# Performance work log

Hardware: AMD Instinct MI355X
Metric: run time of the kernel (lower is better)

## Reference

```python
import jax, jax.numpy as jnp
import numpy as np

DIM = 128
HID = 4 * DIM  # hidden_rate=4
EPS = 1e-5     # torch LayerNorm default


def _ln(x, g, b):
    mu = jnp.mean(x, axis=-1, keepdims=True)
    var = jnp.mean(jnp.square(x - mu), axis=-1, keepdims=True)
    return (x - mu) * jax.lax.rsqrt(var + EPS) * g + b


def setup_inputs() -> dict:
    key = jax.random.key(0)
    ks = jax.random.split(key, 8)
    b, c, h, w = 4, DIM, 128, 128
    inp = {
        'inp_img': jax.random.normal(ks[0], (b, c, h, w), dtype=jnp.float32),
        # layer norms (gamma, beta)
        'ln0_g': jnp.ones((c,), jnp.float32), 'ln0_b': jnp.zeros((c,), jnp.float32),
        'ln1_g': jnp.ones((c,), jnp.float32), 'ln1_b': jnp.zeros((c,), jnp.float32),
        'ln2_g': jnp.ones((c,), jnp.float32), 'ln2_b': jnp.zeros((c,), jnp.float32),
        # SpatialMix output projection (out, in)
        'W_out': jax.random.normal(ks[1], (c, c), jnp.float32) * 0.05,
        # ChannelMix weights
        'W_whiten': jax.random.normal(ks[2], (c, c), jnp.float32) * 0.05,
        'W_key': jax.random.normal(ks[3], (HID, c), jnp.float32) * 0.05,
        'W_recep': jax.random.normal(ks[4], (c, c), jnp.float32) * 0.05,
        'W_value': jax.random.normal(ks[5], (c, HID), jnp.float32) * 0.05,
    }
    return inp


def _block(x, ln0_g, ln0_b, ln1_g, ln1_b, ln2_g, ln2_b,
           W_out, W_whiten, W_key, W_recep, W_value):
    # x: (b, c, h, w) -> tokens (b, T, c)
    b, c, h, w = x.shape
    t = x.reshape(b, c, h * w).transpose(0, 2, 1)
    # layer_id == 0 pre-norm
    t = _ln(t, ln0_g, ln0_b)
    # SpatialMix: jit_func output is discarded (sr overwritten with sigmoid(x));
    # effective math: output_proj(sigmoid(y) * y) on y = ln1(t)
    y1 = _ln(t, ln1_g, ln1_b)
    att = jnp.einsum('btc,oc->bto', jax.nn.sigmoid(y1) * y1, W_out)
    t = t + att
    # ChannelMix: for-else resets xk = xr = whitened x
    y2 = _ln(t, ln2_g, ln2_b)
    wht = jnp.einsum('btc,oc->bto', y2, W_whiten)                 # (b,T,c)
    k = jnp.square(jax.nn.relu(jnp.einsum('btc,hc->bth', wht, W_key)))  # (b,T,HID)
    kv = jnp.einsum('bth,ch->btc', k, W_value)                    # (b,T,c)
    r = jax.nn.sigmoid(jnp.einsum('btc,oc->bto', wht, W_recep))
    t = t + r * kv
    return t.transpose(0, 2, 1).reshape(b, c, h, w)


def reference(inp_img, ln0_g, ln0_b, ln1_g, ln1_b, ln2_g, ln2_b,
              W_out, W_whiten, W_key, W_recep, W_value):
    params = (ln0_g, ln0_b, ln1_g, ln1_b, ln2_g, ln2_b,
              W_out, W_whiten, W_key, W_recep, W_value)
    out1 = _block(inp_img, *params)
    # same encoder applied to h/w-transposed image, then transposed back
    out2 = _block(inp_img.transpose(0, 1, 3, 2), *params).transpose(0, 1, 3, 2)
    return out2 + out1
```

## Files before the change

kernel.cpp:

```cpp
#include <hip/hip_runtime.h>


#define HW    16384
#define CDIM  128
#define LDA   132
#define LDW   136
#define TPW   16
#define NW    16

#define OFF_OUT 0
#define OFF_WHT 16384
#define OFF_KEY 32768
#define OFF_REC 98304
#define OFF_VAL 114688
#define WS_ELEMS 180224

typedef __attribute__((ext_vector_type(8))) short short8;
typedef __attribute__((ext_vector_type(4))) float f32x4;

__device__ __forceinline__ float bf2f(ushort h) {
    union { uint u; float f; } v; v.u = ((uint)h) << 16; return v.f;
}
__device__ __forceinline__ ushort f2bf(float f) {
    union { float f; uint u; } v; v.f = f;
    uint u = v.u + 0x7fffu + ((v.u >> 16) & 1u);
    return (ushort)(u >> 16);
}
__device__ __forceinline__ float sigm(float x) {
    return 1.f / (1.f + __expf(-x));
}

__global__ void cvt_all(const float* __restrict__ Wout, const float* __restrict__ Wwht,
                        const float* __restrict__ Wkey, const float* __restrict__ Wrec,
                        const float* __restrict__ Wval, ushort* __restrict__ ws) {
    int i = blockIdx.x * 256 + threadIdx.x;
    float v;
    if      (i < 32768)  v = (i < 16384) ? Wout[i] : Wwht[i - 16384];
    else if (i < 98304)  v = Wkey[i - 32768];
    else if (i < 114688) v = Wrec[i - 98304];
    else                 v = Wval[i - 114688];
    ws[i] = f2bf(v);
}

template<bool PRE>
__device__ __forceinline__ void stageW(ushort* Wl,
                                       const ushort* __restrict__ wsrc,
                                       const float* __restrict__ fsrc,
                                       int src_ld, int row0, int k0, int tid) {
    const int rr = tid >> 4, cc = (tid & 15) * 8;
#pragma unroll
    for (int j = 0; j < 2; ++j) {
        const int r  = j * 64 + rr;
        const int si = (row0 + r) * src_ld + k0 + cc;
        if (PRE) {
            *(short8*)&Wl[r * LDW + cc] = *(const short8*)&wsrc[si];
        } else {
            const float* p = fsrc + si;
            float4 f0 = *(const float4*)p;
            float4 f1 = *(const float4*)(p + 4);
            union { ushort u[8]; short8 s; } t;
            t.u[0]=f2bf(f0.x); t.u[1]=f2bf(f0.y); t.u[2]=f2bf(f0.z); t.u[3]=f2bf(f0.w);
            t.u[4]=f2bf(f1.x); t.u[5]=f2bf(f1.y); t.u[6]=f2bf(f1.z); t.u[7]=f2bf(f1.w);
            *(short8*)&Wl[r * LDW + cc] = t.s;
        }
    }
}

__device__ __forceinline__ short8 ldA8(const ushort* p) {
    union { uint2 x[2]; short8 s; } r;
    r.x[0] = *(const uint2*)p;
    r.x[1] = *(const uint2*)(p + 4);
    return r.s;
}

__device__ __forceinline__ void gemm16(const ushort* A, const ushort* Wl,
                                       int q, int c, f32x4 acc[8]) {
#pragma unroll
    for (int kk = 0; kk < 4; ++kk) {
        short8 a = ldA8(A + c * LDA + kk * 32 + q * 8);
#pragma unroll
        for (int h = 0; h < 2; ++h) {
            short8 b[4];
#pragma unroll
            for (int g = 0; g < 4; ++g)
                b[g] = *(const short8*)&Wl[((h * 4 + g) * 16 + c) * LDW + kk * 32 + q * 8];
#pragma unroll
            for (int g = 0; g < 4; ++g)
                acc[h * 4 + g] = __builtin_amdgcn_mfma_f32_16x16x32_bf16(
                    a, b[g], acc[h * 4 + g], 0, 0, 0);
        }
    }
}

__device__ __forceinline__ void gemm8r(const short8* wa, const ushort* Wl,
                                       int nt0, int q, int c, f32x4 acc4[4]) {
#pragma unroll
    for (int kk = 0; kk < 4; ++kk) {
        short8 b[4];
#pragma unroll
        for (int g = 0; g < 4; ++g)
            b[g] = *(const short8*)&Wl[((nt0 + g) * 16 + c) * LDW + kk * 32 + q * 8];
#pragma unroll
        for (int g = 0; g < 4; ++g)
            acc4[g] = __builtin_amdgcn_mfma_f32_16x16x32_bf16(
                wa[kk], b[g], acc4[g], 0, 0, 0);
    }
}

__device__ __forceinline__ void zero8(f32x4 a[8]) {
#pragma unroll
    for (int nt = 0; nt < 8; ++nt) a[nt] = (f32x4){0.f, 0.f, 0.f, 0.f};
}
__device__ __forceinline__ void zero4(f32x4 a[4]) {
#pragma unroll
    for (int g = 0; g < 4; ++g) a[g] = (f32x4){0.f, 0.f, 0.f, 0.f};
}

__device__ __forceinline__ void ln_stats(const float* t, float& mu, float& rs) {
    float s1 = 0.f, s2 = 0.f;
#pragma unroll
    for (int i = 0; i < 32; ++i) { s1 += t[i]; s2 += t[i] * t[i]; }
    s1 += __shfl_xor(s1, 16); s2 += __shfl_xor(s2, 16);
    s1 += __shfl_xor(s1, 32); s2 += __shfl_xor(s2, 32);
    mu = s1 * (1.f / 128.f);
    rs = rsqrtf(s2 * (1.f / 128.f) - mu * mu + 1e-5f);
}

template<bool PRE>
__global__ __launch_bounds__(1024, 4) void rwkv_mfma(
    const float* __restrict__ X,
    const float* __restrict__ G0, const float* __restrict__ B0,
    const float* __restrict__ G1, const float* __restrict__ B1,
    const float* __restrict__ G2, const float* __restrict__ B2,
    const float* __restrict__ WoutF, const float* __restrict__ WwhtF,
    const float* __restrict__ WkeyF, const float* __restrict__ WrecF,
    const float* __restrict__ WvalF,
    const ushort* __restrict__ Wb,
    float* __restrict__ Y)
{
    __shared__ __align__(16) ushort actS[NW * TPW * LDA];
    __shared__ __align__(16) ushort WldsA[128 * LDW];
    __shared__ __align__(16) ushort WldsB[128 * LDW];

    const int tid = threadIdx.x;
    const int w = tid >> 6, l = tid & 63;
    const int q = l >> 4, c = l & 15;
    ushort* act = actS + w * (TPW * LDA);

    const int s256 = blockIdx.x * 256;
    const int bb  = s256 >> 14;
    const int s0  = s256 & (HW - 1);
    const long gbase = (long)(bb * CDIM) * HW + s0 + 16 * w + c;

    stageW<PRE>(WldsA, Wb + OFF_OUT, WoutF, 128, 0, 0, tid);

    float t[32];
#pragma unroll
    for (int i = 0; i < 32; ++i) t[i] = X[gbase + (long)(32 * q + i) * HW];

    float mu, rs;
    ln_stats(t, mu, rs);
#pragma unroll
    for (int i = 0; i < 32; ++i) {
        int ch = 32 * q + i;
        t[i] = (t[i] - mu) * rs * G0[ch] + B0[ch];
    }
    ln_stats(t, mu, rs);
#pragma unroll
    for (int j = 0; j < 16; ++j) {
        int ch = 32 * q + 2 * j;
        float y0 = (t[2*j]   - mu) * rs * G1[ch]   + B1[ch];
        float y1 = (t[2*j+1] - mu) * rs * G1[ch+1] + B1[ch+1];
        y0 *= sigm(y0); y1 *= sigm(y1);
        *(uint*)&act[c * LDA + ch] = (uint)f2bf(y0) | ((uint)f2bf(y1) << 16);
    }
    __syncthreads();

    stageW<PRE>(WldsB, Wb + OFF_WHT, WwhtF, 128, 0, 0, tid);
    {
        f32x4 acc[8];
        zero8(acc);
        gemm16(act, WldsA, q, c, acc);
#pragma unroll
        for (int nt = 0; nt < 8; ++nt)
#pragma unroll
            for (int r = 0; r < 4; ++r)
                act[(q * 4 + r) * LDA + nt * 16 + c] = f2bf(acc[nt][r]);
    }
#pragma unroll
    for (int i = 0; i < 32; ++i)
        t[i] += bf2f(act[c * LDA + 32 * q + i]);
    __syncthreads();

    stageW<PRE>(WldsA, Wb + OFF_KEY, WkeyF, 128, 0, 0, tid);
    ln_stats(t, mu, rs);
#pragma unroll
    for (int j = 0; j < 16; ++j) {
        int ch = 32 * q + 2 * j;
        float y0 = (t[2*j]   - mu) * rs * G2[ch]   + B2[ch];
        float y1 = (t[2*j+1] - mu) * rs * G2[ch+1] + B2[ch+1];
        *(uint*)&act[c * LDA + ch] = (uint)f2bf(y0) | ((uint)f2bf(y1) << 16);
    }
    {
        f32x4 acc[8];
        zero8(acc);
        gemm16(act, WldsB, q, c, acc);
#pragma unroll
        for (int nt = 0; nt < 8; ++nt)
#pragma unroll
            for (int r = 0; r < 4; ++r)
                act[(q * 4 + r) * LDA + nt * 16 + c] = f2bf(acc[nt][r]);
    }
    short8 wa[4];
#pragma unroll
    for (int kk = 0; kk < 4; ++kk)
        wa[kk] = ldA8(act + c * LDA + kk * 32 + q * 8);
    __syncthreads();

    f32x4 akv[8];
    zero8(akv);
    for (int chunk = 0; chunk < 4; ++chunk) {
        stageW<PRE>(WldsB, Wb + OFF_VAL, WvalF, 512, 0, chunk * 128, tid);
#pragma unroll
        for (int h = 0; h < 2; ++h) {
            f32x4 a4[4];
            zero4(a4);
            gemm8r(wa, WldsA, h * 4, q, c, a4);
#pragma unroll
            for (int g = 0; g < 4; ++g)
#pragma unroll
                for (int r = 0; r < 4; ++r) {
                    float v = fmaxf(a4[g][r], 0.f);
                    act[(q * 4 + r) * LDA + (h * 4 + g) * 16 + c] = f2bf(v * v);
                }
        }
        __syncthreads();

        if (chunk < 3)
            stageW<PRE>(WldsA, Wb + OFF_KEY, WkeyF, 128, (chunk + 1) * 128, 0, tid);
        else
            stageW<PRE>(WldsA, Wb + OFF_REC, WrecF, 128, 0, 0, tid);
        gemm16(act, WldsB, q, c, akv);
        __syncthreads();
    }

#pragma unroll
    for (int h = 0; h < 2; ++h) {
        f32x4 a4[4];
        zero4(a4);
        gemm8r(wa, WldsA, h * 4, q, c, a4);
#pragma unroll
        for (int g = 0; g < 4; ++g)
#pragma unroll
            for (int r = 0; r < 4; ++r)
                act[(q * 4 + r) * LDA + (h * 4 + g) * 16 + c] =
                    f2bf(sigm(a4[g][r]) * akv[h * 4 + g][r]);
    }

#pragma unroll
    for (int i = 0; i < 32; ++i) {
        float t2 = t[i] + bf2f(act[c * LDA + 32 * q + i]);
        Y[gbase + (long)(32 * q + i) * HW] = 2.f * t2;
    }
}

extern "C" void kernel_launch(void* const* d_in, const int* in_sizes, int n_in,
                              void* d_out, int out_size, void* d_ws, size_t ws_size,
                              hipStream_t stream) {
    (void)in_sizes; (void)n_in; (void)out_size;
    const float* X  = (const float*)d_in[0];
    const float* G0 = (const float*)d_in[1];  const float* B0 = (const float*)d_in[2];
    const float* G1 = (const float*)d_in[3];  const float* B1 = (const float*)d_in[4];
    const float* G2 = (const float*)d_in[5];  const float* B2 = (const float*)d_in[6];
    const float* Wout = (const float*)d_in[7];
    const float* Wwht = (const float*)d_in[8];
    const float* Wkey = (const float*)d_in[9];
    const float* Wrec = (const float*)d_in[10];
    const float* Wval = (const float*)d_in[11];
    float* Y = (float*)d_out;

    const bool pre = ws_size >= (size_t)WS_ELEMS * 2;
    if (pre) {
        ushort* ws = (ushort*)d_ws;
        cvt_all<<<704, 256, 0, stream>>>(Wout, Wwht, Wkey, Wrec, Wval, ws);
        rwkv_mfma<true><<<256, 1024, 0, stream>>>(
            X, G0, B0, G1, B1, G2, B2,
            Wout, Wwht, Wkey, Wrec, Wval, ws, Y);
    } else {
        rwkv_mfma<false><<<256, 1024, 0, stream>>>(
            X, G0, B0, G1, B1, G2, B2,
            Wout, Wwht, Wkey, Wrec, Wval, nullptr, Y);
    }
}
```

Baseline: 153.3 us.

## Use hardware bf16 pack conversion, wider LDS loads, and MFMA priority hints

```diff
diff --git a/kernel.cpp b/kernel.cpp
--- a/kernel.cpp
+++ b/kernel.cpp
@@ -3,7 +3,7 @@
 
 #define HW    16384
 #define CDIM  128
-#define LDA   132
+#define LDA   136
 #define LDW   136
 #define TPW   16
 #define NW    16
@@ -25,6 +25,11 @@
     union { float f; uint u; } v; v.f = f;
     uint u = v.u + 0x7fffu + ((v.u >> 16) & 1u);
     return (ushort)(u >> 16);
+}
+__device__ __forceinline__ uint cvtpk(float a, float b) {
+    uint r;
+    asm("v_cvt_pk_bf16_f32 %0, %1, %2" : "=v"(r) : "v"(a), "v"(b));
+    return r;
 }
 __device__ __forceinline__ float sigm(float x) {
     return 1.f / (1.f + __expf(-x));
@@ -58,26 +63,20 @@
             const float* p = fsrc + si;
             float4 f0 = *(const float4*)p;
             float4 f1 = *(const float4*)(p + 4);
-            union { ushort u[8]; short8 s; } t;
-            t.u[0]=f2bf(f0.x); t.u[1]=f2bf(f0.y); t.u[2]=f2bf(f0.z); t.u[3]=f2bf(f0.w);
-            t.u[4]=f2bf(f1.x); t.u[5]=f2bf(f1.y); t.u[6]=f2bf(f1.z); t.u[7]=f2bf(f1.w);
+            union { uint u[4]; short8 s; } t;
+            t.u[0] = cvtpk(f0.x, f0.y); t.u[1] = cvtpk(f0.z, f0.w);
+            t.u[2] = cvtpk(f1.x, f1.y); t.u[3] = cvtpk(f1.z, f1.w);
             *(short8*)&Wl[r * LDW + cc] = t.s;
         }
     }
 }
 
-__device__ __forceinline__ short8 ldA8(const ushort* p) {
-    union { uint2 x[2]; short8 s; } r;
-    r.x[0] = *(const uint2*)p;
-    r.x[1] = *(const uint2*)(p + 4);
-    return r.s;
-}
-
 __device__ __forceinline__ void gemm16(const ushort* A, const ushort* Wl,
                                        int q, int c, f32x4 acc[8]) {
+    __builtin_amdgcn_s_setprio(1);
 #pragma unroll
     for (int kk = 0; kk < 4; ++kk) {
-        short8 a = ldA8(A + c * LDA + kk * 32 + q * 8);
+        short8 a = *(const short8*)&A[c * LDA + kk * 32 + q * 8];
 #pragma unroll
         for (int h = 0; h < 2; ++h) {
             short8 b[4];
@@ -90,10 +89,12 @@
                     a, b[g], acc[h * 4 + g], 0, 0, 0);
         }
     }
+    __builtin_amdgcn_s_setprio(0);
 }
 
 __device__ __forceinline__ void gemm8r(const short8* wa, const ushort* Wl,
                                        int nt0, int q, int c, f32x4 acc4[4]) {
+    __builtin_amdgcn_s_setprio(1);
 #pragma unroll
     for (int kk = 0; kk < 4; ++kk) {
         short8 b[4];
@@ -105,6 +106,7 @@
             acc4[g] = __builtin_amdgcn_mfma_f32_16x16x32_bf16(
                 wa[kk], b[g], acc4[g], 0, 0, 0);
     }
+    __builtin_amdgcn_s_setprio(0);
 }
 
 __device__ __forceinline__ void zero8(f32x4 a[8]) {
@@ -114,6 +116,15 @@
 __device__ __forceinline__ void zero4(f32x4 a[4]) {
 #pragma unroll
     for (int g = 0; g < 4; ++g) a[g] = (f32x4){0.f, 0.f, 0.f, 0.f};
+}
+
+__device__ __forceinline__ void st4(ushort* dst, int q, int col, const f32x4 v) {
+    uint u01 = cvtpk(v[0], v[1]);
+    uint u23 = cvtpk(v[2], v[3]);
+    dst[(q * 4 + 0) * LDA + col] = (ushort)u01;
+    dst[(q * 4 + 1) * LDA + col] = (ushort)(u01 >> 16);
+    dst[(q * 4 + 2) * LDA + col] = (ushort)u23;
+    dst[(q * 4 + 3) * LDA + col] = (ushort)(u23 >> 16);
 }
 
 __device__ __forceinline__ void ln_stats(const float* t, float& mu, float& rs) {
@@ -172,7 +183,7 @@
         float y0 = (t[2*j]   - mu) * rs * G1[ch]   + B1[ch];
         float y1 = (t[2*j+1] - mu) * rs * G1[ch+1] + B1[ch+1];
         y0 *= sigm(y0); y1 *= sigm(y1);
-        *(uint*)&act[c * LDA + ch] = (uint)f2bf(y0) | ((uint)f2bf(y1) << 16);
+        *(uint*)&act[c * LDA + ch] = cvtpk(y0, y1);
     }
     __syncthreads();
 
@@ -183,9 +194,7 @@
         gemm16(act, WldsA, q, c, acc);
 #pragma unroll
         for (int nt = 0; nt < 8; ++nt)
-#pragma unroll
-            for (int r = 0; r < 4; ++r)
-                act[(q * 4 + r) * LDA + nt * 16 + c] = f2bf(acc[nt][r]);
+            st4(act, q, nt * 16 + c, acc[nt]);
     }
 #pragma unroll
     for (int i = 0; i < 32; ++i)
@@ -199,7 +208,7 @@
         int ch = 32 * q + 2 * j;
         float y0 = (t[2*j]   - mu) * rs * G2[ch]   + B2[ch];
         float y1 = (t[2*j+1] - mu) * rs * G2[ch+1] + B2[ch+1];
-        *(uint*)&act[c * LDA + ch] = (uint)f2bf(y0) | ((uint)f2bf(y1) << 16);
+        *(uint*)&act[c * LDA + ch] = cvtpk(y0, y1);
     }
     {
         f32x4 acc[8];
@@ -207,14 +216,12 @@
         gemm16(act, WldsB, q, c, acc);
 #pragma unroll
         for (int nt = 0; nt < 8; ++nt)
-#pragma unroll
-            for (int r = 0; r < 4; ++r)
-                act[(q * 4 + r) * LDA + nt * 16 + c] = f2bf(acc[nt][r]);
+            st4(act, q, nt * 16 + c, acc[nt]);
     }
     short8 wa[4];
 #pragma unroll
     for (int kk = 0; kk < 4; ++kk)
-        wa[kk] = ldA8(act + c * LDA + kk * 32 + q * 8);
+        wa[kk] = *(const short8*)&act[c * LDA + kk * 32 + q * 8];
     __syncthreads();
 
     f32x4 akv[8];
@@ -227,12 +234,15 @@
             zero4(a4);
             gemm8r(wa, WldsA, h * 4, q, c, a4);
 #pragma unroll
-            for (int g = 0; g < 4; ++g)
+            for (int g = 0; g < 4; ++g) {
+                f32x4 v;
 #pragma unroll
                 for (int r = 0; r < 4; ++r) {
-                    float v = fmaxf(a4[g][r], 0.f);
-                    act[(q * 4 + r) * LDA + (h * 4 + g) * 16 + c] = f2bf(v * v);
+                    float x = fmaxf(a4[g][r], 0.f);
+                    v[r] = x * x;
                 }
+                st4(act, q, (h * 4 + g) * 16 + c, v);
+            }
         }
         __syncthreads();
 
@@ -250,11 +260,13 @@
         zero4(a4);
         gemm8r(wa, WldsA, h * 4, q, c, a4);
 #pragma unroll
-        for (int g = 0; g < 4; ++g)
+        for (int g = 0; g < 4; ++g) {
+            f32x4 v;
 #pragma unroll
             for (int r = 0; r < 4; ++r)
-                act[(q * 4 + r) * LDA + (h * 4 + g) * 16 + c] =
-                    f2bf(sigm(a4[g][r]) * akv[h * 4 + g][r]);
+                v[r] = sigm(a4[g][r]) * akv[h * 4 + g][r];
+            st4(act, q, (h * 4 + g) * 16 + c, v);
+        }
     }
 
 #pragma unroll
```

Result: slower. 162.7 us (+6.1%).
